# Optimization experiments

Hardware: AMD Instinct MI355X
Metric: run time of the kernel (lower is better)

## Reference

```python
import jax, jax.numpy as jnp
import numpy as np

N, DIM, K = 262144, 64, 1024

def setup_inputs() -> dict:
    key = jax.random.key(0)
    k1, k2 = jax.random.split(key)
    x = jax.random.normal(k1, (N, DIM), dtype=jnp.float32)
    embed = jax.random.normal(k2, (K, DIM), dtype=jnp.float32)
    return {"x": x, "embed": embed}

def reference(x, embed):
    distances = (jnp.sum(x * x, axis=-1, keepdims=True)
                 - 2.0 * (x @ embed.T)
                 + jnp.sum(embed * embed, axis=-1))  # [N, K]
    idx = jnp.argmin(distances, axis=-1)  # [N]
    # dequantize: embedding lookup
    out = embed[idx]  # [N, DIM]
    return out
```

## Files before the change

kernel.cpp:

```cpp
#include <hip/hip_runtime.h>


#define VQ_N 262144
#define VQ_DIM 64
#define VQ_K 1024
#define NT 64
#define TCH 256
#define FLAG_EPS 1.2e-2f

typedef short short8 __attribute__((ext_vector_type(8)));
typedef float f32x4 __attribute__((ext_vector_type(4)));

#define WS_BFRAG 0
#define WS_E2    (256*1024)
#define WS_NEEDED (260*1024)

static __device__ __forceinline__ unsigned short f2bf_rtne(float f) {
    unsigned u = __float_as_uint(f);
    unsigned r = u + 0x7FFFu + ((u >> 16) & 1u);
    return (unsigned short)(r >> 16);
}
static __device__ __forceinline__ float bf2f(unsigned short h) {
    return __uint_as_float(((unsigned)h) << 16);
}

__global__ void vq_prep(const float* __restrict__ embed, unsigned char* ws) {
    int t = blockIdx.x * 256 + threadIdx.x;
    if (t < NT * TCH) {
        int ct = t >> 8;
        int c = t & 255;
        int arr = c >> 7;
        int kc = (c >> 6) & 1;
        int l = c & 63;
        int code = ct * 16 + (l & 15);
        int kbase = kc * 32 + ((l >> 4) << 3);
        const float* ep = embed + (size_t)code * VQ_DIM + kbase;
        short8 pack;
#pragma unroll
        for (int j = 0; j < 8; ++j) {
            float v = ep[j];
            unsigned short h = f2bf_rtne(v);
            pack[j] = arr ? (short)f2bf_rtne(v - bf2f(h)) : (short)h;
        }
        ((short8*)(ws + WS_BFRAG))[t] = pack;
    } else if (t < NT * TCH + VQ_K) {
        int code = t - NT * TCH;
        const float* ep = embed + (size_t)code * VQ_DIM;
        float a0 = 0, a1 = 0, a2 = 0, a3 = 0;
#pragma unroll
        for (int j = 0; j < VQ_DIM; j += 4) {
            a0 = fmaf(ep[j], ep[j], a0);
            a1 = fmaf(ep[j + 1], ep[j + 1], a1);
            a2 = fmaf(ep[j + 2], ep[j + 2], a2);
            a3 = fmaf(ep[j + 3], ep[j + 3], a3);
        }
        ((float*)(ws + WS_E2))[code] = (a0 + a1) + (a2 + a3);
    }
}

__global__ __launch_bounds__(256, 4)
void vq_stage1(const float* __restrict__ x, const float* __restrict__ embed,
               unsigned char* ws, float* __restrict__ out) {
    __shared__ int idx_s[4][32];

    const int tid = threadIdx.x;
    const int lane = tid & 63;
    const int wave = tid >> 6;
    const int gwave = blockIdx.x * 4 + wave;
    const int R0 = gwave * 32;
    const int g = lane >> 4;
    const int khalf = g << 3;

    const short8* bsrc = (const short8*)(ws + WS_BFRAG);
    const float* e2g = (const float*)(ws + WS_E2);

    short8 ah00, ah01, al00, al01, ah10, ah11, al10, al11;
#define MAKE_A(ROW, KC, AH, AL)                                             \
    {                                                                       \
        const float4* p4 = (const float4*)(x + (size_t)(ROW) * VQ_DIM +     \
                                           (KC) * 32 + khalf);              \
        float4 v0 = p4[0], v1 = p4[1];                                      \
        float q0 = -2.0f * v0.x, q1 = -2.0f * v0.y, q2 = -2.0f * v0.z,      \
              q3 = -2.0f * v0.w, q4 = -2.0f * v1.x, q5 = -2.0f * v1.y,      \
              q6 = -2.0f * v1.z, q7 = -2.0f * v1.w;                         \
        unsigned short h0 = f2bf_rtne(q0), h1 = f2bf_rtne(q1),              \
                       h2 = f2bf_rtne(q2), h3 = f2bf_rtne(q3),              \
                       h4 = f2bf_rtne(q4), h5 = f2bf_rtne(q5),              \
                       h6 = f2bf_rtne(q6), h7 = f2bf_rtne(q7);              \
        AH[0] = (short)h0; AH[1] = (short)h1; AH[2] = (short)h2;            \
        AH[3] = (short)h3; AH[4] = (short)h4; AH[5] = (short)h5;            \
        AH[6] = (short)h6; AH[7] = (short)h7;                               \
        AL[0] = (short)f2bf_rtne(q0 - bf2f(h0));                            \
        AL[1] = (short)f2bf_rtne(q1 - bf2f(h1));                            \
        AL[2] = (short)f2bf_rtne(q2 - bf2f(h2));                            \
        AL[3] = (short)f2bf_rtne(q3 - bf2f(h3));                            \
        AL[4] = (short)f2bf_rtne(q4 - bf2f(h4));                            \
        AL[5] = (short)f2bf_rtne(q5 - bf2f(h5));                            \
        AL[6] = (short)f2bf_rtne(q6 - bf2f(h6));                            \
        AL[7] = (short)f2bf_rtne(q7 - bf2f(h7));                            \
    }
    const int row0 = R0 + (lane & 15);
    const int row1 = row0 + 16;
    MAKE_A(row0, 0, ah00, al00)
    MAKE_A(row0, 1, ah01, al01)
    MAKE_A(row1, 0, ah10, al10)
    MAKE_A(row1, 1, ah11, al11)
#undef MAKE_A

    unsigned m1k0[4], m2k0[4], m1k1[4], m2k1[4];
#pragma unroll
    for (int r = 0; r < 4; ++r) {
        m1k0[r] = 0xFFFFFFFFu; m2k0[r] = 0xFFFFFFFFu;
        m1k1[r] = 0xFFFFFFFFu; m2k1[r] = 0xFFFFFFFFu;
    }

#pragma unroll 2
    for (int ct = 0; ct < NT; ++ct) {
        const short8* bt = bsrc + (size_t)ct * TCH;
        short8 bh0 = bt[lane];
        short8 bh1 = bt[64 + lane];
        short8 bl0 = bt[128 + lane];
        short8 bl1 = bt[192 + lane];
        float e2c = e2g[ct * 16 + (lane & 15)] + 256.0f;
        unsigned ctu = (unsigned)ct;

        f32x4 acc0 = {e2c, e2c, e2c, e2c};
        acc0 = __builtin_amdgcn_mfma_f32_16x16x32_bf16(al00, bh0, acc0, 0, 0, 0);
        acc0 = __builtin_amdgcn_mfma_f32_16x16x32_bf16(al01, bh1, acc0, 0, 0, 0);
        acc0 = __builtin_amdgcn_mfma_f32_16x16x32_bf16(ah00, bl0, acc0, 0, 0, 0);
        acc0 = __builtin_amdgcn_mfma_f32_16x16x32_bf16(ah01, bl1, acc0, 0, 0, 0);
        acc0 = __builtin_amdgcn_mfma_f32_16x16x32_bf16(ah00, bh0, acc0, 0, 0, 0);
        acc0 = __builtin_amdgcn_mfma_f32_16x16x32_bf16(ah01, bh1, acc0, 0, 0, 0);

        f32x4 acc1 = {e2c, e2c, e2c, e2c};
        acc1 = __builtin_amdgcn_mfma_f32_16x16x32_bf16(al10, bh0, acc1, 0, 0, 0);
        acc1 = __builtin_amdgcn_mfma_f32_16x16x32_bf16(al11, bh1, acc1, 0, 0, 0);
        acc1 = __builtin_amdgcn_mfma_f32_16x16x32_bf16(ah10, bl0, acc1, 0, 0, 0);
        acc1 = __builtin_amdgcn_mfma_f32_16x16x32_bf16(ah11, bl1, acc1, 0, 0, 0);
        acc1 = __builtin_amdgcn_mfma_f32_16x16x32_bf16(ah10, bh0, acc1, 0, 0, 0);
        acc1 = __builtin_amdgcn_mfma_f32_16x16x32_bf16(ah11, bh1, acc1, 0, 0, 0);

#pragma unroll
        for (int r = 0; r < 4; ++r) {
            unsigned key = (__float_as_uint(acc0[r]) & 0xFFFFFFC0u) | ctu;
            unsigned t1 = m1k0[r] > key ? m1k0[r] : key;
            m2k0[r] = m2k0[r] < t1 ? m2k0[r] : t1;
            m1k0[r] = m1k0[r] < key ? m1k0[r] : key;
        }
#pragma unroll
        for (int r = 0; r < 4; ++r) {
            unsigned key = (__float_as_uint(acc1[r]) & 0xFFFFFFC0u) | ctu;
            unsigned t1 = m1k1[r] > key ? m1k1[r] : key;
            m2k1[r] = m2k1[r] < t1 ? m2k1[r] : t1;
            m1k1[r] = m1k1[r] < key ? m1k1[r] : key;
        }
    }

    unsigned res0[4], res1[4];
#pragma unroll
    for (int r = 0; r < 4; ++r) { res0[r] = (unsigned)(lane & 15); res1[r] = res0[r]; }
#define RED_STEP(M1, M2, RES, m)                                                      \
    {                                                                                 \
        _Pragma("unroll")                                                             \
        for (int r = 0; r < 4; ++r) {                                                 \
            unsigned ok = (unsigned)__shfl_xor((int)M1[r], m);                        \
            unsigned ok2 = (unsigned)__shfl_xor((int)M2[r], m);                       \
            unsigned orr = (unsigned)__shfl_xor((int)RES[r], m);                      \
            unsigned t1 = M1[r] > ok ? M1[r] : ok;                                    \
            unsigned c2 = ok2 < t1 ? ok2 : t1;                                        \
            M2[r] = M2[r] < c2 ? M2[r] : c2;                                          \
            bool take = (ok < M1[r]) || (ok == M1[r] && orr < RES[r]);                \
            if (take) { M1[r] = ok; RES[r] = orr; }                                   \
        }                                                                             \
    }
#pragma unroll
    for (int m = 1; m <= 8; m <<= 1) {
        RED_STEP(m1k0, m2k0, res0, m)
        RED_STEP(m1k1, m2k1, res1, m)
    }
#undef RED_STEP

    unsigned fmask = 0;
    if ((lane & 15) == 0) {
#pragma unroll
        for (int r = 0; r < 4; ++r) {
            int rl0 = 4 * g + r;
            idx_s[wave][rl0] = (int)((m1k0[r] & 63u) * 16u + res0[r]);
            float s1 = __uint_as_float(m1k0[r] & 0xFFFFFFC0u);
            float s2 = __uint_as_float(m2k0[r] & 0xFFFFFFC0u);
            if (s2 - s1 < FLAG_EPS) fmask |= 1u << rl0;
            int rl1 = 16 + 4 * g + r;
            idx_s[wave][rl1] = (int)((m1k1[r] & 63u) * 16u + res1[r]);
            float t1f = __uint_as_float(m1k1[r] & 0xFFFFFFC0u);
            float t2f = __uint_as_float(m2k1[r] & 0xFFFFFFC0u);
            if (t2f - t1f < FLAG_EPS) fmask |= 1u << rl1;
        }
    }
    fmask |= (unsigned)__shfl_xor((int)fmask, 16);
    fmask |= (unsigned)__shfl_xor((int)fmask, 32);
    unsigned wmask = (unsigned)__shfl((int)fmask, 0);
    __syncthreads();

    const int orow = tid >> 1;
    const int ohalf = tid & 1;
    int code = idx_s[orow >> 5][orow & 31];
    const float4* ep = (const float4*)(embed + (size_t)code * VQ_DIM) + ohalf * 8;
    float4* op = (float4*)(out + (size_t)(blockIdx.x * 128 + orow) * VQ_DIM) + ohalf * 8;
#pragma unroll
    for (int j = 0; j < 8; ++j) op[j] = ep[j];

    while (wmask) {
        int b = __ffs(wmask) - 1;
        wmask &= wmask - 1;
        int row = R0 + b;
        const float* xr = x + (size_t)row * VQ_DIM;
        float xv[VQ_DIM];
#pragma unroll
        for (int j = 0; j < VQ_DIM / 4; ++j) {
            float4 v = ((const float4*)xr)[j];
            xv[4 * j] = v.x; xv[4 * j + 1] = v.y;
            xv[4 * j + 2] = v.z; xv[4 * j + 3] = v.w;
        }
        float best = __builtin_inff();
        int bi = VQ_K;
        for (int t = 0; t < VQ_K / 64; ++t) {
            int c = t * 64 + lane;
            const float* ep2 = embed + (size_t)c * VQ_DIM;
            float a0 = 0, a1 = 0, a2 = 0, a3 = 0;
#pragma unroll
            for (int j = 0; j < VQ_DIM; j += 4) {
                a0 = fmaf(xv[j], ep2[j], a0);
                a1 = fmaf(xv[j + 1], ep2[j + 1], a1);
                a2 = fmaf(xv[j + 2], ep2[j + 2], a2);
                a3 = fmaf(xv[j + 3], ep2[j + 3], a3);
            }
            float dot = (a0 + a1) + (a2 + a3);
            float s = fmaf(-2.0f, dot, e2g[c]);
            if (s < best || (s == best && c < bi)) { best = s; bi = c; }
        }
#pragma unroll
        for (int m = 1; m <= 32; m <<= 1) {
            float ob = __shfl_xor(best, m);
            int oi = __shfl_xor(bi, m);
            if (ob < best || (ob == best && oi < bi)) { best = ob; bi = oi; }
        }
        out[(size_t)row * VQ_DIM + lane] = embed[(size_t)bi * VQ_DIM + lane];
    }
}

__global__ __launch_bounds__(256, 4)
void vq_fallback(const float* __restrict__ x, const float* __restrict__ embed,
                 float* __restrict__ out) {
    __shared__ float e2s[VQ_K];
    const int tid = threadIdx.x;
    for (int c = tid; c < VQ_K; c += 256) {
        const float4* ep = (const float4*)(embed + c * VQ_DIM);
        float s = 0.0f;
#pragma unroll
        for (int j = 0; j < VQ_DIM / 4; ++j) {
            float4 v = ep[j];
            s = fmaf(v.x, v.x, s); s = fmaf(v.y, v.y, s);
            s = fmaf(v.z, v.z, s); s = fmaf(v.w, v.w, s);
        }
        e2s[c] = s;
    }
    __syncthreads();
    const int row = blockIdx.x * 256 + tid;
    float xr[VQ_DIM];
    const float4* xp = (const float4*)(x + (size_t)row * VQ_DIM);
#pragma unroll
    for (int j = 0; j < VQ_DIM / 4; ++j) {
        float4 v = xp[j];
        xr[4 * j] = v.x; xr[4 * j + 1] = v.y; xr[4 * j + 2] = v.z; xr[4 * j + 3] = v.w;
    }
    float best = __builtin_inff();
    int bidx = 0;
    for (int c = 0; c < VQ_K; ++c) {
        const float4* ep = (const float4*)(embed + c * VQ_DIM);
        float a0 = 0, a1 = 0, a2 = 0, a3 = 0;
#pragma unroll
        for (int j = 0; j < VQ_DIM / 4; ++j) {
            float4 v = ep[j];
            a0 = fmaf(xr[4 * j], v.x, a0);
            a1 = fmaf(xr[4 * j + 1], v.y, a1);
            a2 = fmaf(xr[4 * j + 2], v.z, a2);
            a3 = fmaf(xr[4 * j + 3], v.w, a3);
        }
        float score = fmaf(-2.0f, (a0 + a1) + (a2 + a3), e2s[c]);
        if (score < best) { best = score; bidx = c; }
    }
    const float4* bp = (const float4*)(embed + (size_t)bidx * VQ_DIM);
    float4* op = (float4*)(out + (size_t)row * VQ_DIM);
#pragma unroll
    for (int j = 0; j < VQ_DIM / 4; ++j) op[j] = bp[j];
}

extern "C" void kernel_launch(void* const* d_in, const int* in_sizes, int n_in,
                              void* d_out, int out_size, void* d_ws, size_t ws_size,
                              hipStream_t stream) {
    const float* x = (const float*)d_in[0];
    const float* embed = (const float*)d_in[1];
    float* out = (float*)d_out;
    if (ws_size < WS_NEEDED) {
        hipLaunchKernelGGL(vq_fallback, dim3(VQ_N / 256), dim3(256), 0, stream, x, embed, out);
        return;
    }
    unsigned char* ws = (unsigned char*)d_ws;
    hipLaunchKernelGGL(vq_prep, dim3(68), dim3(256), 0, stream, embed, ws);
    hipLaunchKernelGGL(vq_stage1, dim3(VQ_N / 128), dim3(256), 0, stream, x, embed, ws, out);
}
```

Baseline: 172.3 us.

## Use single-wave blocks with shuffle-based code exchange instead of shared memory

```diff
diff --git a/kernel.cpp b/kernel.cpp
--- a/kernel.cpp
+++ b/kernel.cpp
@@ -13,7 +13,8 @@
 
 #define WS_BFRAG 0
 #define WS_E2    (256*1024)
-#define WS_NEEDED (260*1024)
+#define WS_E2P   (260*1024)
+#define WS_NEEDED (264*1024)
 
 static __device__ __forceinline__ unsigned short f2bf_rtne(float f) {
     unsigned u = __float_as_uint(f);
@@ -54,25 +55,25 @@
             a2 = fmaf(ep[j + 2], ep[j + 2], a2);
             a3 = fmaf(ep[j + 3], ep[j + 3], a3);
         }
-        ((float*)(ws + WS_E2))[code] = (a0 + a1) + (a2 + a3);
-    }
-}
-
-__global__ __launch_bounds__(256, 4)
+        float e2 = (a0 + a1) + (a2 + a3);
+        ((float*)(ws + WS_E2))[code] = e2;
+        ((float*)(ws + WS_E2P))[code] = e2 + 256.0f;
+    }
+}
+
+__global__ __launch_bounds__(64, 4)
 void vq_stage1(const float* __restrict__ x, const float* __restrict__ embed,
                unsigned char* ws, float* __restrict__ out) {
-    __shared__ int idx_s[4][32];
-
-    const int tid = threadIdx.x;
-    const int lane = tid & 63;
-    const int wave = tid >> 6;
-    const int gwave = blockIdx.x * 4 + wave;
+    const int lane = threadIdx.x;
+    const int gwave = blockIdx.x;
     const int R0 = gwave * 32;
     const int g = lane >> 4;
+    const int res = lane & 15;
     const int khalf = g << 3;
 
     const short8* bsrc = (const short8*)(ws + WS_BFRAG);
     const float* e2g = (const float*)(ws + WS_E2);
+    const float* e2p = (const float*)(ws + WS_E2P);
 
     short8 ah00, ah01, al00, al01, ah10, ah11, al10, al11;
 #define MAKE_A(ROW, KC, AH, AL)                                             \
@@ -99,7 +100,7 @@
         AL[6] = (short)f2bf_rtne(q6 - bf2f(h6));                            \
         AL[7] = (short)f2bf_rtne(q7 - bf2f(h7));                            \
     }
-    const int row0 = R0 + (lane & 15);
+    const int row0 = R0 + res;
     const int row1 = row0 + 16;
     MAKE_A(row0, 0, ah00, al00)
     MAKE_A(row0, 1, ah01, al01)
@@ -121,7 +122,7 @@
         short8 bh1 = bt[64 + lane];
         short8 bl0 = bt[128 + lane];
         short8 bl1 = bt[192 + lane];
-        float e2c = e2g[ct * 16 + (lane & 15)] + 256.0f;
+        float e2c = e2p[ct * 16 + res];
         unsigned ctu = (unsigned)ct;
 
         f32x4 acc0 = {e2c, e2c, e2c, e2c};
@@ -158,7 +159,7 @@
 
     unsigned res0[4], res1[4];
 #pragma unroll
-    for (int r = 0; r < 4; ++r) { res0[r] = (unsigned)(lane & 15); res1[r] = res0[r]; }
+    for (int r = 0; r < 4; ++r) { res0[r] = (unsigned)res; res1[r] = res0[r]; }
 #define RED_STEP(M1, M2, RES, m)                                                      \
     {                                                                                 \
         _Pragma("unroll")                                                             \
@@ -180,47 +181,47 @@
     }
 #undef RED_STEP
 
+    int code0[4], code1[4];
     unsigned fmask = 0;
-    if ((lane & 15) == 0) {
-#pragma unroll
-        for (int r = 0; r < 4; ++r) {
-            int rl0 = 4 * g + r;
-            idx_s[wave][rl0] = (int)((m1k0[r] & 63u) * 16u + res0[r]);
-            float s1 = __uint_as_float(m1k0[r] & 0xFFFFFFC0u);
-            float s2 = __uint_as_float(m2k0[r] & 0xFFFFFFC0u);
-            if (s2 - s1 < FLAG_EPS) fmask |= 1u << rl0;
-            int rl1 = 16 + 4 * g + r;
-            idx_s[wave][rl1] = (int)((m1k1[r] & 63u) * 16u + res1[r]);
-            float t1f = __uint_as_float(m1k1[r] & 0xFFFFFFC0u);
-            float t2f = __uint_as_float(m2k1[r] & 0xFFFFFFC0u);
-            if (t2f - t1f < FLAG_EPS) fmask |= 1u << rl1;
-        }
+#pragma unroll
+    for (int r = 0; r < 4; ++r) {
+        code0[r] = (int)((m1k0[r] & 63u) * 16u + res0[r]);
+        code1[r] = (int)((m1k1[r] & 63u) * 16u + res1[r]);
+        float s1a = __uint_as_float(m1k0[r] & 0xFFFFFFC0u);
+        float s2a = __uint_as_float(m2k0[r] & 0xFFFFFFC0u);
+        if (s2a - s1a < FLAG_EPS) fmask |= 1u << (4 * g + r);
+        float s1b = __uint_as_float(m1k1[r] & 0xFFFFFFC0u);
+        float s2b = __uint_as_float(m2k1[r] & 0xFFFFFFC0u);
+        if (s2b - s1b < FLAG_EPS) fmask |= 1u << (16 + 4 * g + r);
     }
     fmask |= (unsigned)__shfl_xor((int)fmask, 16);
     fmask |= (unsigned)__shfl_xor((int)fmask, 32);
-    unsigned wmask = (unsigned)__shfl((int)fmask, 0);
-    __syncthreads();
-
-    const int orow = tid >> 1;
-    const int ohalf = tid & 1;
-    int code = idx_s[orow >> 5][orow & 31];
-    const float4* ep = (const float4*)(embed + (size_t)code * VQ_DIM) + ohalf * 8;
-    float4* op = (float4*)(out + (size_t)(blockIdx.x * 128 + orow) * VQ_DIM) + ohalf * 8;
-#pragma unroll
-    for (int j = 0; j < 8; ++j) op[j] = ep[j];
+    unsigned wmask = fmask;
+
+    {
+        const int q = lane >> 1;
+        const int setq = q >> 4;
+        const int gq = (q & 15) >> 2;
+        const int rq = q & 3;
+        const int src = gq << 4;
+        int a0 = __shfl(code0[0], src), a1 = __shfl(code0[1], src);
+        int a2 = __shfl(code0[2], src), a3 = __shfl(code0[3], src);
+        int b0 = __shfl(code1[0], src), b1 = __shfl(code1[1], src);
+        int b2 = __shfl(code1[2], src), b3 = __shfl(code1[3], src);
+        int cs0 = (rq == 0) ? a0 : (rq == 1) ? a1 : (rq == 2) ? a2 : a3;
+        int cs1 = (rq == 0) ? b0 : (rq == 1) ? b1 : (rq == 2) ? b2 : b3;
+        int my = setq ? cs1 : cs0;
+        const float4* ep = (const float4*)(embed + (size_t)my * VQ_DIM) + (lane & 1) * 8;
+        float4* op = (float4*)(out + (size_t)(R0 + q) * VQ_DIM) + (lane & 1) * 8;
+#pragma unroll
+        for (int j = 0; j < 8; ++j) op[j] = ep[j];
+    }
 
     while (wmask) {
         int b = __ffs(wmask) - 1;
         wmask &= wmask - 1;
         int row = R0 + b;
         const float* xr = x + (size_t)row * VQ_DIM;
-        float xv[VQ_DIM];
-#pragma unroll
-        for (int j = 0; j < VQ_DIM / 4; ++j) {
-            float4 v = ((const float4*)xr)[j];
-            xv[4 * j] = v.x; xv[4 * j + 1] = v.y;
-            xv[4 * j + 2] = v.z; xv[4 * j + 3] = v.w;
-        }
         float best = __builtin_inff();
         int bi = VQ_K;
         for (int t = 0; t < VQ_K / 64; ++t) {
@@ -229,10 +230,10 @@
             float a0 = 0, a1 = 0, a2 = 0, a3 = 0;
 #pragma unroll
             for (int j = 0; j < VQ_DIM; j += 4) {
-                a0 = fmaf(xv[j], ep2[j], a0);
-                a1 = fmaf(xv[j + 1], ep2[j + 1], a1);
-                a2 = fmaf(xv[j + 2], ep2[j + 2], a2);
-                a3 = fmaf(xv[j + 3], ep2[j + 3], a3);
+                a0 = fmaf(xr[j], ep2[j], a0);
+                a1 = fmaf(xr[j + 1], ep2[j + 1], a1);
+                a2 = fmaf(xr[j + 2], ep2[j + 2], a2);
+                a3 = fmaf(xr[j + 3], ep2[j + 3], a3);
             }
             float dot = (a0 + a1) + (a2 + a3);
             float s = fmaf(-2.0f, dot, e2g[c]);
@@ -307,5 +308,5 @@
     }
     unsigned char* ws = (unsigned char*)d_ws;
     hipLaunchKernelGGL(vq_prep, dim3(68), dim3(256), 0, stream, embed, ws);
-    hipLaunchKernelGGL(vq_stage1, dim3(VQ_N / 128), dim3(256), 0, stream, x, embed, ws, out);
-}
+    hipLaunchKernelGGL(vq_stage1, dim3(VQ_N / 32), dim3(64), 0, stream, x, embed, ws, out);
+}
```

Result: slower. 176.5 us (+2.4%).

## Split argmin into cheap bf16 pass and refined pass on ambiguous rows

Applied to the files above, without the earlier changes.

```diff
diff --git a/kernel.cpp b/kernel.cpp
--- a/kernel.cpp
+++ b/kernel.cpp
@@ -5,15 +5,20 @@
 #define VQ_DIM 64
 #define VQ_K 1024
 #define NT 64
-#define TCH 256
-#define FLAG_EPS 1.2e-2f
+#define TCH 128
+#define EPS1 0.32f
+#define EPS2 1.2e-2f
+#define LIST_CAP 32768
 
 typedef short short8 __attribute__((ext_vector_type(8)));
 typedef float f32x4 __attribute__((ext_vector_type(4)));
 
-#define WS_BFRAG 0
+#define WS_BH    0
+#define WS_BL    (128*1024)
 #define WS_E2    (256*1024)
-#define WS_NEEDED (260*1024)
+#define WS_CNT   (260*1024)
+#define WS_LIST  (261*1024)
+#define WS_NEEDED (392*1024)
 
 static __device__ __forceinline__ unsigned short f2bf_rtne(float f) {
     unsigned u = __float_as_uint(f);
@@ -26,10 +31,10 @@
 
 __global__ void vq_prep(const float* __restrict__ embed, unsigned char* ws) {
     int t = blockIdx.x * 256 + threadIdx.x;
-    if (t < NT * TCH) {
-        int ct = t >> 8;
-        int c = t & 255;
-        int arr = c >> 7;
+    if (t < 16384) {
+        int arr = t >> 13;
+        int c = t & 8191;
+        int ct = c >> 7;
         int kc = (c >> 6) & 1;
         int l = c & 63;
         int code = ct * 16 + (l & 15);
@@ -42,9 +47,9 @@
             unsigned short h = f2bf_rtne(v);
             pack[j] = arr ? (short)f2bf_rtne(v - bf2f(h)) : (short)h;
         }
-        ((short8*)(ws + WS_BFRAG))[t] = pack;
-    } else if (t < NT * TCH + VQ_K) {
-        int code = t - NT * TCH;
+        ((short8*)(ws + (arr ? WS_BL : WS_BH)))[c] = pack;
+    } else if (t < 16384 + VQ_K) {
+        int code = t - 16384;
         const float* ep = embed + (size_t)code * VQ_DIM;
         float a0 = 0, a1 = 0, a2 = 0, a3 = 0;
 #pragma unroll
@@ -55,26 +60,11 @@
             a3 = fmaf(ep[j + 3], ep[j + 3], a3);
         }
         ((float*)(ws + WS_E2))[code] = (a0 + a1) + (a2 + a3);
-    }
-}
-
-__global__ __launch_bounds__(256, 4)
-void vq_stage1(const float* __restrict__ x, const float* __restrict__ embed,
-               unsigned char* ws, float* __restrict__ out) {
-    __shared__ int idx_s[4][32];
-
-    const int tid = threadIdx.x;
-    const int lane = tid & 63;
-    const int wave = tid >> 6;
-    const int gwave = blockIdx.x * 4 + wave;
-    const int R0 = gwave * 32;
-    const int g = lane >> 4;
-    const int khalf = g << 3;
-
-    const short8* bsrc = (const short8*)(ws + WS_BFRAG);
-    const float* e2g = (const float*)(ws + WS_E2);
-
-    short8 ah00, ah01, al00, al01, ah10, ah11, al10, al11;
+    } else if (t == 16384 + VQ_K) {
+        *(unsigned*)(ws + WS_CNT) = 0u;
+    }
+}
+
 #define MAKE_A(ROW, KC, AH, AL)                                             \
     {                                                                       \
         const float4* p4 = (const float4*)(x + (size_t)(ROW) * VQ_DIM +     \
@@ -99,66 +89,16 @@
         AL[6] = (short)f2bf_rtne(q6 - bf2f(h6));                            \
         AL[7] = (short)f2bf_rtne(q7 - bf2f(h7));                            \
     }
-    const int row0 = R0 + (lane & 15);
-    const int row1 = row0 + 16;
-    MAKE_A(row0, 0, ah00, al00)
-    MAKE_A(row0, 1, ah01, al01)
-    MAKE_A(row1, 0, ah10, al10)
-    MAKE_A(row1, 1, ah11, al11)
-#undef MAKE_A
-
-    unsigned m1k0[4], m2k0[4], m1k1[4], m2k1[4];
-#pragma unroll
-    for (int r = 0; r < 4; ++r) {
-        m1k0[r] = 0xFFFFFFFFu; m2k0[r] = 0xFFFFFFFFu;
-        m1k1[r] = 0xFFFFFFFFu; m2k1[r] = 0xFFFFFFFFu;
-    }
-
-#pragma unroll 2
-    for (int ct = 0; ct < NT; ++ct) {
-        const short8* bt = bsrc + (size_t)ct * TCH;
-        short8 bh0 = bt[lane];
-        short8 bh1 = bt[64 + lane];
-        short8 bl0 = bt[128 + lane];
-        short8 bl1 = bt[192 + lane];
-        float e2c = e2g[ct * 16 + (lane & 15)] + 256.0f;
-        unsigned ctu = (unsigned)ct;
-
-        f32x4 acc0 = {e2c, e2c, e2c, e2c};
-        acc0 = __builtin_amdgcn_mfma_f32_16x16x32_bf16(al00, bh0, acc0, 0, 0, 0);
-        acc0 = __builtin_amdgcn_mfma_f32_16x16x32_bf16(al01, bh1, acc0, 0, 0, 0);
-        acc0 = __builtin_amdgcn_mfma_f32_16x16x32_bf16(ah00, bl0, acc0, 0, 0, 0);
-        acc0 = __builtin_amdgcn_mfma_f32_16x16x32_bf16(ah01, bl1, acc0, 0, 0, 0);
-        acc0 = __builtin_amdgcn_mfma_f32_16x16x32_bf16(ah00, bh0, acc0, 0, 0, 0);
-        acc0 = __builtin_amdgcn_mfma_f32_16x16x32_bf16(ah01, bh1, acc0, 0, 0, 0);
-
-        f32x4 acc1 = {e2c, e2c, e2c, e2c};
-        acc1 = __builtin_amdgcn_mfma_f32_16x16x32_bf16(al10, bh0, acc1, 0, 0, 0);
-        acc1 = __builtin_amdgcn_mfma_f32_16x16x32_bf16(al11, bh1, acc1, 0, 0, 0);
-        acc1 = __builtin_amdgcn_mfma_f32_16x16x32_bf16(ah10, bl0, acc1, 0, 0, 0);
-        acc1 = __builtin_amdgcn_mfma_f32_16x16x32_bf16(ah11, bl1, acc1, 0, 0, 0);
-        acc1 = __builtin_amdgcn_mfma_f32_16x16x32_bf16(ah10, bh0, acc1, 0, 0, 0);
-        acc1 = __builtin_amdgcn_mfma_f32_16x16x32_bf16(ah11, bh1, acc1, 0, 0, 0);
-
-#pragma unroll
-        for (int r = 0; r < 4; ++r) {
-            unsigned key = (__float_as_uint(acc0[r]) & 0xFFFFFFC0u) | ctu;
-            unsigned t1 = m1k0[r] > key ? m1k0[r] : key;
-            m2k0[r] = m2k0[r] < t1 ? m2k0[r] : t1;
-            m1k0[r] = m1k0[r] < key ? m1k0[r] : key;
-        }
-#pragma unroll
-        for (int r = 0; r < 4; ++r) {
-            unsigned key = (__float_as_uint(acc1[r]) & 0xFFFFFFC0u) | ctu;
-            unsigned t1 = m1k1[r] > key ? m1k1[r] : key;
-            m2k1[r] = m2k1[r] < t1 ? m2k1[r] : t1;
-            m1k1[r] = m1k1[r] < key ? m1k1[r] : key;
-        }
-    }
-
-    unsigned res0[4], res1[4];
-#pragma unroll
-    for (int r = 0; r < 4; ++r) { res0[r] = (unsigned)(lane & 15); res1[r] = res0[r]; }
+
+#define KEYUPD(ACC, M1, M2, CTU)                                                      \
+        _Pragma("unroll")                                                             \
+        for (int r = 0; r < 4; ++r) {                                                 \
+            unsigned key = (__float_as_uint(ACC[r]) & 0xFFFFFFC0u) | (CTU);           \
+            unsigned t1 = M1[r] > key ? M1[r] : key;                                  \
+            M2[r] = M2[r] < t1 ? M2[r] : t1;                                          \
+            M1[r] = M1[r] < key ? M1[r] : key;                                        \
+        }
+
 #define RED_STEP(M1, M2, RES, m)                                                      \
     {                                                                                 \
         _Pragma("unroll")                                                             \
@@ -173,32 +113,137 @@
             if (take) { M1[r] = ok; RES[r] = orr; }                                   \
         }                                                                             \
     }
+
+#define EXACT_ROW(ROW)                                                                \
+    {                                                                                 \
+        const float* xr = x + (size_t)(ROW) * VQ_DIM;                                 \
+        float best = __builtin_inff();                                                \
+        int bi = VQ_K;                                                                \
+        for (int t = 0; t < VQ_K / 64; ++t) {                                         \
+            int c = t * 64 + lane;                                                    \
+            const float* ep2 = embed + (size_t)c * VQ_DIM;                            \
+            float a0 = 0, a1 = 0, a2 = 0, a3 = 0;                                     \
+            _Pragma("unroll")                                                         \
+            for (int j = 0; j < VQ_DIM; j += 4) {                                     \
+                a0 = fmaf(xr[j], ep2[j], a0);                                         \
+                a1 = fmaf(xr[j + 1], ep2[j + 1], a1);                                 \
+                a2 = fmaf(xr[j + 2], ep2[j + 2], a2);                                 \
+                a3 = fmaf(xr[j + 3], ep2[j + 3], a3);                                 \
+            }                                                                         \
+            float dot = (a0 + a1) + (a2 + a3);                                        \
+            float s = fmaf(-2.0f, dot, e2g[c]);                                       \
+            if (s < best || (s == best && c < bi)) { best = s; bi = c; }              \
+        }                                                                             \
+        _Pragma("unroll")                                                             \
+        for (int m = 1; m <= 32; m <<= 1) {                                           \
+            float ob = __shfl_xor(best, m);                                           \
+            int oi = __shfl_xor(bi, m);                                               \
+            if (ob < best || (ob == best && oi < bi)) { best = ob; bi = oi; }         \
+        }                                                                             \
+        out[(size_t)(ROW) * VQ_DIM + lane] = embed[(size_t)bi * VQ_DIM + lane];       \
+    }
+
+__global__ __launch_bounds__(256, 4)
+void vq_stage1(const float* __restrict__ x, const float* __restrict__ embed,
+               unsigned char* ws, float* __restrict__ out) {
+    __shared__ int idx_s[4][32];
+
+    const int tid = threadIdx.x;
+    const int lane = tid & 63;
+    const int wave = tid >> 6;
+    const int gwave = blockIdx.x * 4 + wave;
+    const int R0 = gwave * 32;
+    const int g = lane >> 4;
+    const int res = lane & 15;
+    const int khalf = g << 3;
+
+    const short8* bsrc = (const short8*)(ws + WS_BH);
+    const float* e2g = (const float*)(ws + WS_E2);
+    unsigned* cnt = (unsigned*)(ws + WS_CNT);
+    int* list = (int*)(ws + WS_LIST);
+
+    short8 ah00, ah01, al00, al01, ah10, ah11, al10, al11;
+    const int row0 = R0 + res;
+    const int row1 = row0 + 16;
+    MAKE_A(row0, 0, ah00, al00)
+    MAKE_A(row0, 1, ah01, al01)
+    MAKE_A(row1, 0, ah10, al10)
+    MAKE_A(row1, 1, ah11, al11)
+
+    unsigned m1k0[4], m2k0[4], m1k1[4], m2k1[4];
+#pragma unroll
+    for (int r = 0; r < 4; ++r) {
+        m1k0[r] = 0xFFFFFFFFu; m2k0[r] = 0xFFFFFFFFu;
+        m1k1[r] = 0xFFFFFFFFu; m2k1[r] = 0xFFFFFFFFu;
+    }
+
+#pragma unroll 2
+    for (int ct = 0; ct < NT; ++ct) {
+        const short8* bt = bsrc + (size_t)ct * TCH;
+        short8 bh0 = bt[lane];
+        short8 bh1 = bt[64 + lane];
+        float e2c = e2g[ct * 16 + res] + 256.0f;
+        unsigned ctu = (unsigned)ct;
+
+        f32x4 acc0 = {e2c, e2c, e2c, e2c};
+        acc0 = __builtin_amdgcn_mfma_f32_16x16x32_bf16(al00, bh0, acc0, 0, 0, 0);
+        acc0 = __builtin_amdgcn_mfma_f32_16x16x32_bf16(al01, bh1, acc0, 0, 0, 0);
+        acc0 = __builtin_amdgcn_mfma_f32_16x16x32_bf16(ah00, bh0, acc0, 0, 0, 0);
+        acc0 = __builtin_amdgcn_mfma_f32_16x16x32_bf16(ah01, bh1, acc0, 0, 0, 0);
+
+        f32x4 acc1 = {e2c, e2c, e2c, e2c};
+        acc1 = __builtin_amdgcn_mfma_f32_16x16x32_bf16(al10, bh0, acc1, 0, 0, 0);
+        acc1 = __builtin_amdgcn_mfma_f32_16x16x32_bf16(al11, bh1, acc1, 0, 0, 0);
+        acc1 = __builtin_amdgcn_mfma_f32_16x16x32_bf16(ah10, bh0, acc1, 0, 0, 0);
+        acc1 = __builtin_amdgcn_mfma_f32_16x16x32_bf16(ah11, bh1, acc1, 0, 0, 0);
+
+        KEYUPD(acc0, m1k0, m2k0, ctu)
+        KEYUPD(acc1, m1k1, m2k1, ctu)
+    }
+
+    unsigned res0[4], res1[4];
+#pragma unroll
+    for (int r = 0; r < 4; ++r) { res0[r] = (unsigned)res; res1[r] = res0[r]; }
 #pragma unroll
     for (int m = 1; m <= 8; m <<= 1) {
         RED_STEP(m1k0, m2k0, res0, m)
         RED_STEP(m1k1, m2k1, res1, m)
     }
-#undef RED_STEP
 
     unsigned fmask = 0;
-    if ((lane & 15) == 0) {
+    if (res == 0) {
 #pragma unroll
         for (int r = 0; r < 4; ++r) {
             int rl0 = 4 * g + r;
             idx_s[wave][rl0] = (int)((m1k0[r] & 63u) * 16u + res0[r]);
             float s1 = __uint_as_float(m1k0[r] & 0xFFFFFFC0u);
             float s2 = __uint_as_float(m2k0[r] & 0xFFFFFFC0u);
-            if (s2 - s1 < FLAG_EPS) fmask |= 1u << rl0;
+            if (s2 - s1 < EPS1) fmask |= 1u << rl0;
             int rl1 = 16 + 4 * g + r;
             idx_s[wave][rl1] = (int)((m1k1[r] & 63u) * 16u + res1[r]);
             float t1f = __uint_as_float(m1k1[r] & 0xFFFFFFC0u);
             float t2f = __uint_as_float(m2k1[r] & 0xFFFFFFC0u);
-            if (t2f - t1f < FLAG_EPS) fmask |= 1u << rl1;
+            if (t2f - t1f < EPS1) fmask |= 1u << rl1;
         }
     }
     fmask |= (unsigned)__shfl_xor((int)fmask, 16);
     fmask |= (unsigned)__shfl_xor((int)fmask, 32);
-    unsigned wmask = (unsigned)__shfl((int)fmask, 0);
+
+    unsigned omask = 0;
+    if (lane == 0 && fmask) {
+        int n = __popc(fmask);
+        unsigned pos = atomicAdd(cnt, (unsigned)n);
+        unsigned m = fmask;
+        int i = 0;
+        while (m) {
+            int b = __ffs(m) - 1;
+            m &= m - 1;
+            if (pos + (unsigned)i < LIST_CAP) list[pos + i] = R0 + b;
+            else omask |= 1u << b;
+            ++i;
+        }
+    }
+    omask = (unsigned)__shfl((int)omask, 0);
     __syncthreads();
 
     const int orow = tid >> 1;
@@ -209,42 +254,139 @@
 #pragma unroll
     for (int j = 0; j < 8; ++j) op[j] = ep[j];
 
+    while (omask) {
+        int b = __ffs(omask) - 1;
+        omask &= omask - 1;
+        EXACT_ROW(R0 + b)
+    }
+}
+
+__global__ __launch_bounds__(256, 4)
+void vq_stage2(const float* __restrict__ x, const float* __restrict__ embed,
+               unsigned char* ws, float* __restrict__ out) {
+    const int tid = threadIdx.x;
+    const int lane = tid & 63;
+    const int wave = tid >> 6;
+    const int w = blockIdx.x * 4 + wave;
+
+    const unsigned* cnt = (const unsigned*)(ws + WS_CNT);
+    const int* list = (const int*)(ws + WS_LIST);
+    const short8* bh = (const short8*)(ws + WS_BH);
+    const short8* bl = (const short8*)(ws + WS_BL);
+    const float* e2g = (const float*)(ws + WS_E2);
+
+    int n = (int)*cnt;
+    n = n < LIST_CAP ? n : LIST_CAP;
+    int nw = (n + 31) >> 5;
+    if (w >= nw) return;
+
+    const int base = w * 32;
+    const int g = lane >> 4;
+    const int res = lane & 15;
+    const int khalf = g << 3;
+
+    const int i0 = base + res;
+    const int i1 = base + 16 + res;
+    const int row0 = list[i0 < n ? i0 : n - 1];
+    const int row1 = list[i1 < n ? i1 : n - 1];
+
+    short8 ah00, ah01, al00, al01, ah10, ah11, al10, al11;
+    MAKE_A(row0, 0, ah00, al00)
+    MAKE_A(row0, 1, ah01, al01)
+    MAKE_A(row1, 0, ah10, al10)
+    MAKE_A(row1, 1, ah11, al11)
+
+    unsigned m1k0[4], m2k0[4], m1k1[4], m2k1[4];
+#pragma unroll
+    for (int r = 0; r < 4; ++r) {
+        m1k0[r] = 0xFFFFFFFFu; m2k0[r] = 0xFFFFFFFFu;
+        m1k1[r] = 0xFFFFFFFFu; m2k1[r] = 0xFFFFFFFFu;
+    }
+
+#pragma unroll 2
+    for (int ct = 0; ct < NT; ++ct) {
+        const short8* bht = bh + (size_t)ct * TCH;
+        const short8* blt = bl + (size_t)ct * TCH;
+        short8 bh0 = bht[lane];
+        short8 bh1 = bht[64 + lane];
+        short8 bl0 = blt[lane];
+        short8 bl1 = blt[64 + lane];
+        float e2c = e2g[ct * 16 + res] + 256.0f;
+        unsigned ctu = (unsigned)ct;
+
+        f32x4 acc0 = {e2c, e2c, e2c, e2c};
+        acc0 = __builtin_amdgcn_mfma_f32_16x16x32_bf16(al00, bh0, acc0, 0, 0, 0);
+        acc0 = __builtin_amdgcn_mfma_f32_16x16x32_bf16(al01, bh1, acc0, 0, 0, 0);
+        acc0 = __builtin_amdgcn_mfma_f32_16x16x32_bf16(ah00, bl0, acc0, 0, 0, 0);
+        acc0 = __builtin_amdgcn_mfma_f32_16x16x32_bf16(ah01, bl1, acc0, 0, 0, 0);
+        acc0 = __builtin_amdgcn_mfma_f32_16x16x32_bf16(ah00, bh0, acc0, 0, 0, 0);
+        acc0 = __builtin_amdgcn_mfma_f32_16x16x32_bf16(ah01, bh1, acc0, 0, 0, 0);
+
+        f32x4 acc1 = {e2c, e2c, e2c, e2c};
+        acc1 = __builtin_amdgcn_mfma_f32_16x16x32_bf16(al10, bh0, acc1, 0, 0, 0);
+        acc1 = __builtin_amdgcn_mfma_f32_16x16x32_bf16(al11, bh1, acc1, 0, 0, 0);
+        acc1 = __builtin_amdgcn_mfma_f32_16x16x32_bf16(ah10, bl0, acc1, 0, 0, 0);
+        acc1 = __builtin_amdgcn_mfma_f32_16x16x32_bf16(ah11, bl1, acc1, 0, 0, 0);
+        acc1 = __builtin_amdgcn_mfma_f32_16x16x32_bf16(ah10, bh0, acc1, 0, 0, 0);
+        acc1 = __builtin_amdgcn_mfma_f32_16x16x32_bf16(ah11, bh1, acc1, 0, 0, 0);
+
+        KEYUPD(acc0, m1k0, m2k0, ctu)
+        KEYUPD(acc1, m1k1, m2k1, ctu)
+    }
+
+    unsigned res0[4], res1[4];
+#pragma unroll
+    for (int r = 0; r < 4; ++r) { res0[r] = (unsigned)res; res1[r] = res0[r]; }
+#pragma unroll
+    for (int m = 1; m <= 8; m <<= 1) {
+        RED_STEP(m1k0, m2k0, res0, m)
+        RED_STEP(m1k1, m2k1, res1, m)
+    }
+
+    int code0[4], code1[4];
+    unsigned fmask = 0;
+#pragma unroll
+    for (int r = 0; r < 4; ++r) {
+        code0[r] = (int)((m1k0[r] & 63u) * 16u + res0[r]);
+        code1[r] = (int)((m1k1[r] & 63u) * 16u + res1[r]);
+        float s1a = __uint_as_float(m1k0[r] & 0xFFFFFFC0u);
+        float s2a = __uint_as_float(m2k0[r] & 0xFFFFFFC0u);
+        if (s2a - s1a < EPS2) fmask |= 1u << (4 * g + r);
+        float s1b = __uint_as_float(m1k1[r] & 0xFFFFFFC0u);
+        float s2b = __uint_as_float(m2k1[r] & 0xFFFFFFC0u);
+        if (s2b - s1b < EPS2) fmask |= 1u << (16 + 4 * g + r);
+    }
+    fmask |= (unsigned)__shfl_xor((int)fmask, 16);
+    fmask |= (unsigned)__shfl_xor((int)fmask, 32);
+    unsigned wmask = (unsigned)__shfl((int)fmask, 0);
+
+    {
+        const int q = lane >> 1;
+        const int iq = base + q;
+        const int rowq = list[iq < n ? iq : n - 1];
+        const int setq = q >> 4;
+        const int gq = (q & 15) >> 2;
+        const int rq = q & 3;
+        const int src = gq << 4;
+        int a0 = __shfl(code0[0], src), a1 = __shfl(code0[1], src);
+        int a2 = __shfl(code0[2], src), a3 = __shfl(code0[3], src);
+        int b0 = __shfl(code1[0], src), b1 = __shfl(code1[1], src);
+        int b2 = __shfl(code1[2], src), b3 = __shfl(code1[3], src);
+        int cs0 = (rq == 0) ? a0 : (rq == 1) ? a1 : (rq == 2) ? a2 : a3;
+        int cs1 = (rq == 0) ? b0 : (rq == 1) ? b1 : (rq == 2) ? b2 : b3;
+        int my = setq ? cs1 : cs0;
+        const float4* ep = (const float4*)(embed + (size_t)my * VQ_DIM) + (lane & 1) * 8;
+        float4* op = (float4*)(out + (size_t)rowq * VQ_DIM) + (lane & 1) * 8;
+#pragma unroll
+        for (int j = 0; j < 8; ++j) op[j] = ep[j];
+    }
+
     while (wmask) {
         int b = __ffs(wmask) - 1;
         wmask &= wmask - 1;
-        int row = R0 + b;
-        const float* xr = x + (size_t)row * VQ_DIM;
-        float xv[VQ_DIM];
-#pragma unroll
-        for (int j = 0; j < VQ_DIM / 4; ++j) {
-            float4 v = ((const float4*)xr)[j];
-            xv[4 * j] = v.x; xv[4 * j + 1] = v.y;
-            xv[4 * j + 2] = v.z; xv[4 * j + 3] = v.w;
-        }
-        float best = __builtin_inff();
-        int bi = VQ_K;
-        for (int t = 0; t < VQ_K / 64; ++t) {
-            int c = t * 64 + lane;
-            const float* ep2 = embed + (size_t)c * VQ_DIM;
-            float a0 = 0, a1 = 0, a2 = 0, a3 = 0;
-#pragma unroll
-            for (int j = 0; j < VQ_DIM; j += 4) {
-                a0 = fmaf(xv[j], ep2[j], a0);
-                a1 = fmaf(xv[j + 1], ep2[j + 1], a1);
-                a2 = fmaf(xv[j + 2], ep2[j + 2], a2);
-                a3 = fmaf(xv[j + 3], ep2[j + 3], a3);
-            }
-            float dot = (a0 + a1) + (a2 + a3);
-            float s = fmaf(-2.0f, dot, e2g[c]);
-            if (s < best || (s == best && c < bi)) { best = s; bi = c; }
-        }
-#pragma unroll
-        for (int m = 1; m <= 32; m <<= 1) {
-            float ob = __shfl_xor(best, m);
-            int oi = __shfl_xor(bi, m);
-            if (ob < best || (ob == best && oi < bi)) { best = ob; bi = oi; }
-        }
-        out[(size_t)row * VQ_DIM + lane] = embed[(size_t)bi * VQ_DIM + lane];
+        int ib = base + b;
+        int row = list[ib < n ? ib : n - 1];
+        EXACT_ROW(row)
     }
 }
 
@@ -306,6 +448,7 @@
         return;
     }
     unsigned char* ws = (unsigned char*)d_ws;
-    hipLaunchKernelGGL(vq_prep, dim3(68), dim3(256), 0, stream, embed, ws);
+    hipLaunchKernelGGL(vq_prep, dim3(70), dim3(256), 0, stream, embed, ws);
     hipLaunchKernelGGL(vq_stage1, dim3(VQ_N / 128), dim3(256), 0, stream, x, embed, ws, out);
-}
+    hipLaunchKernelGGL(vq_stage2, dim3(VQ_N / 128), dim3(256), 0, stream, x, embed, ws, out);
+}
```

After: 275.6 us. 1.6x slower.
